# Optimization experiments

Measured on AMD Instinct MI355X. Metric: run time of the kernel, lower is better.

Reference implementation:

```python
import jax, jax.numpy as jnp
import numpy as np

N = 50000
E = 400000
IN_DIM = 384
HID = 256
Q_DIM = 384
HEAD_HID = 128


def _glorot(key, shape):
    fan_in, fan_out = shape[0], shape[1]
    lim = float(np.sqrt(6.0 / (fan_in + fan_out)))
    return jax.random.uniform(key, shape, jnp.float32, -lim, lim)


def setup_inputs() -> dict:
    key = jax.random.key(0)
    ks = jax.random.split(key, 10)
    x = jax.random.normal(ks[0], (N, IN_DIM), jnp.float32)
    edge_index = jax.random.randint(ks[1], (2, E), 0, N, dtype=jnp.int64)
    q = jax.random.normal(ks[2], (Q_DIM,), jnp.float32)
    # layer 1: Linear(in_dim*2 + query_dim -> hidden)
    W1 = _glorot(ks[3], (IN_DIM * 2 + Q_DIM, HID))
    b1 = jnp.zeros((HID,), jnp.float32)
    # layer 2: Linear(hidden*2 + query_dim -> hidden)
    W2 = _glorot(ks[4], (HID * 2 + Q_DIM, HID))
    b2 = jnp.zeros((HID,), jnp.float32)
    # score head: Linear(hidden + query_dim -> 128) -> ReLU -> Linear(128 -> 1)
    Wh1 = _glorot(ks[5], (HID + Q_DIM, HEAD_HID))
    bh1 = jnp.zeros((HEAD_HID,), jnp.float32)
    Wh2 = _glorot(ks[6], (HEAD_HID, 1))
    bh2 = jnp.zeros((1,), jnp.float32)
    return {"x": x, "edge_index": edge_index, "q": q,
            "W1": W1, "b1": b1, "W2": W2, "b2": b2,
            "Wh1": Wh1, "bh1": bh1, "Wh2": Wh2, "bh2": bh2}


def _sage_layer(h, src, dst, q, W, b, n_nodes):
    # mean aggregation with self-loops: (sum_{j in N(i)} h_j + h_i) / (deg_i + 1)
    deg = jnp.zeros((n_nodes,), h.dtype).at[dst].add(1.0) + 1.0  # [N]
    agg = (jax.ops.segment_sum(h[src], dst, num_segments=n_nodes) + h) / deg[:, None]
    q_exp = jnp.broadcast_to(q, (n_nodes, q.shape[0]))
    cat = jnp.concatenate([h, agg, q_exp], axis=-1)  # [N, 2*d + q_dim]
    return jax.nn.relu(cat @ W + b)  # dropout is identity in eval mode


def reference(x, edge_index, q, W1, b1, W2, b2, Wh1, bh1, Wh2, bh2):
    src, dst = edge_index[0], edge_index[1]
    n = x.shape[0]
    h = _sage_layer(x, src, dst, q, W1, b1, n)
    h = _sage_layer(h, src, dst, q, W2, b2, n)
    q_exp = jnp.broadcast_to(q, (n, q.shape[0]))
    s = jax.nn.relu(jnp.concatenate([h, q_exp], axis=-1) @ Wh1 + bh1)
    logits = (s @ Wh2 + bh2).squeeze(-1)  # [N]
    return logits
```

## Files before the change

kernel.cpp:

```cpp
#include <hip/hip_runtime.h>
#include <cstdint>
#include <cstddef>

typedef unsigned short u16;
typedef short short8 __attribute__((ext_vector_type(8)));
typedef unsigned short u16x8 __attribute__((ext_vector_type(8)));
typedef unsigned short u16x4 __attribute__((ext_vector_type(4)));
typedef float f32x4 __attribute__((ext_vector_type(4)));

#define DEVI __device__ __forceinline__

#if defined(__has_builtin)
#if __has_builtin(__builtin_amdgcn_global_load_lds)
#define USE_GLD 1
#endif
#endif

DEVI float bf2f(u16 u) { return __uint_as_float(((unsigned)u) << 16); }
DEVI u16 f2bf(float f) {
  unsigned u = __float_as_uint(f);
  u += 0x7FFFu + ((u >> 16) & 1u);
  return (u16)(u >> 16);
}

DEVI void stage16(const u16* __restrict__ g, u16* lds_base, int lane) {
#ifdef USE_GLD
  __builtin_amdgcn_global_load_lds(
      (const __attribute__((address_space(1))) unsigned int*)g,
      (__attribute__((address_space(3))) unsigned int*)lds_base, 16, 0, 0);
#else
  *(u16x8*)(lds_base + lane * 8) = *(const u16x8*)g;
#endif
}

__global__ void build_deg(const int* __restrict__ dst, int* __restrict__ deg, int E) {
  int e = blockIdx.x * 256 + threadIdx.x;
  if (e < E) atomicAdd(&deg[dst[e]], 1);
}

__global__ __launch_bounds__(256) void scan1(const int* __restrict__ deg,
                                             int* __restrict__ pref,
                                             int* __restrict__ bsum, int Nn) {
  __shared__ int wsum[4];
  int i = blockIdx.x * 256 + threadIdx.x;
  int lane = threadIdx.x & 63, w = threadIdx.x >> 6;
  int v = (i < Nn) ? deg[i] : 0;
  int s = v;
  for (int off = 1; off < 64; off <<= 1) {
    int t = __shfl_up(s, off, 64);
    if (lane >= off) s += t;
  }
  if (lane == 63) wsum[w] = s;
  __syncthreads();
  int add = 0;
  for (int k = 0; k < w; ++k) add += wsum[k];
  int incl = s + add;
  if (i < Nn) pref[i] = incl - v;
  if (threadIdx.x == 255) bsum[blockIdx.x] = incl;
}

__global__ __launch_bounds__(256) void scan2(int* __restrict__ bsum,
                                             int* __restrict__ row_ofs,
                                             int nb, int Nn) {
  __shared__ int wsum[4];
  int t = threadIdx.x;
  int lane = t & 63, w = t >> 6;
  int v = (t < nb) ? bsum[t] : 0;
  int s = v;
  for (int off = 1; off < 64; off <<= 1) {
    int u = __shfl_up(s, off, 64);
    if (lane >= off) s += u;
  }
  if (lane == 63) wsum[w] = s;
  __syncthreads();
  int add = 0;
  for (int k = 0; k < w; ++k) add += wsum[k];
  int incl = s + add;
  if (t < nb) bsum[t] = incl - v;
  if (t == 255) row_ofs[Nn] = incl;
}

__global__ __launch_bounds__(256) void scan3(const int* __restrict__ pref,
                                             const int* __restrict__ bsum,
                                             int* __restrict__ row_ofs,
                                             int* __restrict__ cursor, int Nn) {
  int i = blockIdx.x * 256 + threadIdx.x;
  if (i < Nn) {
    int r = pref[i] + bsum[blockIdx.x];
    row_ofs[i] = r;
    cursor[i] = r;
  }
}

__global__ void csr_fill(const int* __restrict__ src, const int* __restrict__ dst,
                         int* __restrict__ cursor, int* __restrict__ col, int E) {
  int e = blockIdx.x * 256 + threadIdx.x;
  if (e < E) {
    int p = atomicAdd(&cursor[dst[e]], 1);
    col[p] = src[e];
  }
}

__global__ __launch_bounds__(256) void pack_all(
    const float* __restrict__ W1, const float* __restrict__ W2,
    const float* __restrict__ Wh1, u16* __restrict__ B1t,
    u16* __restrict__ B2t, u16* __restrict__ Bht) {
  int b = blockIdx.x;
  if (b < 1024) {
    int c = b >> 1;
    int k = (b & 1) * 256 + threadIdx.x;
    if (k < 384) {
      float v = (c < 256) ? W1[(size_t)k * 256 + c]
                          : W1[(size_t)(384 + k) * 256 + (c - 256)];
      B1t[(size_t)c * 384 + k] = f2bf(v);
    }
  } else if (b < 1536) {
    int c = b - 1024;
    int k = threadIdx.x;
    float v = (c < 256) ? W2[(size_t)k * 256 + c]
                        : W2[(size_t)(256 + k) * 256 + (c - 256)];
    B2t[(size_t)c * 256 + k] = f2bf(v);
  } else {
    int c = b - 1536;
    int k = threadIdx.x;
    Bht[(size_t)c * 256 + k] = f2bf(Wh1[(size_t)k * 128 + c]);
  }
}

__global__ __launch_bounds__(384) void bias_all(
    const float* __restrict__ W1, const float* __restrict__ b1,
    const float* __restrict__ W2, const float* __restrict__ b2,
    const float* __restrict__ Wh1, const float* __restrict__ bh1,
    const float* __restrict__ q, float* __restrict__ cq1,
    float* __restrict__ cq2, float* __restrict__ cqh) {
  __shared__ float part[6];
  int b = blockIdx.x;
  const float* W; const float* bb; float* o; int ld, roff, c;
  if (b < 256)      { W = W1;  bb = b1;  o = cq1; ld = 256; roff = 768; c = b; }
  else if (b < 512) { W = W2;  bb = b2;  o = cq2; ld = 256; roff = 512; c = b - 256; }
  else              { W = Wh1; bb = bh1; o = cqh; ld = 128; roff = 256; c = b - 512; }
  int t = threadIdx.x;
  float p = q[t] * W[(size_t)(roff + t) * ld + c];
  for (int off = 32; off > 0; off >>= 1) p += __shfl_down(p, off, 64);
  if ((t & 63) == 0) part[t >> 6] = p;
  __syncthreads();
  if (t == 0) {
    float acc = bb[c];
    for (int w = 0; w < 6; ++w) acc += part[w];
    o[c] = acc;
  }
}

#define W_NC 512
#define ES 520
#define OFF_A0 0
#define OFF_A1 (64 * 32)
#define OFF_B0 (2 * 64 * 32)
#define OFF_B1 (2 * 64 * 32 + 512 * 32)
#define SMEM_TOT (2 * 64 * 32 + 2 * 512 * 32)

#define GEMM512_COMPUTE(LA, LB)                                                \
  {                                                                            \
    short8 bfr[8];                                                             \
    _Pragma("unroll") for (int nt = 0; nt < 8; ++nt) bfr[nt] =                 \
        *(const short8*)&(LB)[((wave * 128 + nt * 16 + m) * 4 + csel) * 8];    \
    _Pragma("unroll") for (int mt = 0; mt < 4; ++mt) {                         \
      short8 af = *(const short8*)&(LA)[((mt * 16 + m) * 4 + csel) * 8];       \
      _Pragma("unroll") for (int nt = 0; nt < 8; ++nt)                         \
          acc[mt][nt] = __builtin_amdgcn_mfma_f32_16x16x32_bf16(               \
              af, bfr[nt], acc[mt][nt], 0, 0, 0);                              \
    }                                                                          \
  }

#define GEMM512_EPILOGUE()                                                     \
  {                                                                            \
    u16* et = lds_b0;                                                          \
    _Pragma("unroll") for (int mt = 0; mt < 4; ++mt) {                         \
      __syncthreads();                                                         \
      _Pragma("unroll") for (int nt = 0; nt < 8; ++nt) {                       \
        int col = wave * 128 + nt * 16 + m;                                    \
        float bb = (col < bias_len) ? bias[col] : 0.0f;                        \
        _Pragma("unroll") for (int r = 0; r < 4; ++r) {                        \
          float v = acc[mt][nt][r] + bb;                                       \
          if (relu) v = fmaxf(v, 0.0f);                                        \
          et[(quad * 4 + r) * ES + col] = f2bf(v);                             \
        }                                                                      \
      }                                                                        \
      __syncthreads();                                                         \
      _Pragma("unroll") for (int p = 0; p < 4; ++p) {                          \
        int row_loc = p * 4 + wave;                                            \
        int grow = row0 + mt * 16 + row_loc;                                   \
        if (grow < M)                                                          \
          *(u16x8*)&C[(size_t)grow * W_NC + lane * 8] =                        \
              *(const u16x8*)&et[row_loc * ES + lane * 8];                     \
      }                                                                        \
    }                                                                          \
  }

#define GEMM512_B_SETUP()                                                      \
  const u16* pbB[8];                                                           \
  _Pragma("unroll") for (int p = 0; p < 8; ++p) {                              \
    int L = p * 256 + tid;                                                     \
    int c = L >> 2, qs = L & 3;                                                \
    int g = qs ^ ((c >> 1) & 3);                                               \
    pbB[p] = Bt + (size_t)c * K + g * 8;                                       \
  }

#define GEMM512_B_STAGE2()                                                     \
  _Pragma("unroll") for (int p = 0; p < 8; ++p) {                              \
    u16* d = lds_b0 + (size_t)(p * 256 + wave * 64) * 8;                       \
    stage16(pbB[p], d, lane);                                                  \
    stage16(pbB[p] + 32, d + (512 * 32), lane);         \
    pbB[p] += 64;                                                              \
  }

__global__ __launch_bounds__(256, 2) void gemm512_f32a(
    const float* __restrict__ A, const u16* __restrict__ Bt,
    u16* __restrict__ C, const float* __restrict__ bias,
    int M, int K, int bias_len, int relu) {
  __shared__ __align__(16) u16 smem[SMEM_TOT];
  u16* lds_a0 = smem + OFF_A0;
  u16* lds_a1 = smem + OFF_A1;
  u16* lds_b0 = smem + OFF_B0;
  u16* lds_b1 = smem + OFF_B1;

  const int tid = threadIdx.x;
  const int lane = tid & 63;
  const int wave = tid >> 6;
  const int row0 = blockIdx.x * 64;
  const int m = lane & 15;
  const int quad = lane >> 4;
  const int csel = quad ^ ((m >> 1) & 3);

  const int rA = tid >> 2;
  const int qA = tid & 3;
  const int sA = rA * 4 + (qA ^ ((rA >> 1) & 3));
  int ga = row0 + rA; if (ga >= M) ga = M - 1;
  const float* pa = A + (size_t)ga * K + qA * 8;

  GEMM512_B_SETUP()

  f32x4 acc[4][8] = {};

  f32x4 v0a = *(const f32x4*)pa, v0b = *(const f32x4*)(pa + 4);
  f32x4 v1a = *(const f32x4*)(pa + 32), v1b = *(const f32x4*)(pa + 36);
  pa += 64;

  for (int k0 = 0; k0 < K; k0 += 64) {
    __syncthreads();
    GEMM512_B_STAGE2()
    u16x8 h0, h1;
#pragma unroll
    for (int j = 0; j < 4; ++j) {
      h0[j] = f2bf(v0a[j]); h0[j + 4] = f2bf(v0b[j]);
      h1[j] = f2bf(v1a[j]); h1[j + 4] = f2bf(v1b[j]);
    }
    *(u16x8*)&lds_a0[sA * 8] = h0;
    *(u16x8*)&lds_a1[sA * 8] = h1;
    const float* pn = (k0 + 64 < K) ? pa : A;
    f32x4 n0a = *(const f32x4*)pn, n0b = *(const f32x4*)(pn + 4);
    f32x4 n1a = *(const f32x4*)(pn + 32), n1b = *(const f32x4*)(pn + 36);
    pa += 64;
    __syncthreads();
    GEMM512_COMPUTE(lds_a0, lds_b0)
    GEMM512_COMPUTE(lds_a1, lds_b1)
    v0a = n0a; v0b = n0b; v1a = n1a; v1b = n1b;
  }

  GEMM512_EPILOGUE()
}

__global__ __launch_bounds__(256, 2) void gemm512_bf16a(
    const u16* __restrict__ A, const u16* __restrict__ Bt,
    u16* __restrict__ C, const float* __restrict__ bias,
    int M, int K, int bias_len, int relu) {
  __shared__ __align__(16) u16 smem[SMEM_TOT];
  u16* lds_a0 = smem + OFF_A0;
  u16* lds_a1 = smem + OFF_A1;
  u16* lds_b0 = smem + OFF_B0;
  u16* lds_b1 = smem + OFF_B1;

  const int tid = threadIdx.x;
  const int lane = tid & 63;
  const int wave = tid >> 6;
  const int row0 = blockIdx.x * 64;
  const int m = lane & 15;
  const int quad = lane >> 4;
  const int csel = quad ^ ((m >> 1) & 3);

  const int rA = tid >> 2;
  const int qA = tid & 3;
  const int sA = rA * 4 + (qA ^ ((rA >> 1) & 3));
  int ga = row0 + rA; if (ga >= M) ga = M - 1;
  const u16* pa = A + (size_t)ga * K + qA * 8;

  GEMM512_B_SETUP()

  f32x4 acc[4][8] = {};

  u16x8 va0 = *(const u16x8*)pa;
  u16x8 va1 = *(const u16x8*)(pa + 32);
  pa += 64;

  for (int k0 = 0; k0 < K; k0 += 64) {
    __syncthreads();
    GEMM512_B_STAGE2()
    *(u16x8*)&lds_a0[sA * 8] = va0;
    *(u16x8*)&lds_a1[sA * 8] = va1;
    const u16* pn = (k0 + 64 < K) ? pa : A;
    u16x8 na0 = *(const u16x8*)pn;
    u16x8 na1 = *(const u16x8*)(pn + 32);
    pa += 64;
    __syncthreads();
    GEMM512_COMPUTE(lds_a0, lds_b0)
    GEMM512_COMPUTE(lds_a1, lds_b1)
    va0 = na0; va1 = na1;
  }

  GEMM512_EPILOGUE()
}

#define BM 128
#define BK 32

__global__ __launch_bounds__(256) void gemm_head(
    const u16* __restrict__ A, const u16* __restrict__ Bt,
    const float* __restrict__ cqh, const float* __restrict__ Wh2,
    const float* __restrict__ bh2, float* __restrict__ out, int M, int K) {
  __shared__ __align__(16) u16 lds_a[BM * BK];
  __shared__ __align__(16) u16 lds_b[BM * BK];
  __shared__ float red[128][2];

  const int tid = threadIdx.x;
  const int lane = tid & 63;
  const int wave = tid >> 6;
  const int wm = wave & 1, wn = wave >> 1;
  const int row0 = blockIdx.x * BM;
  const int m = lane & 15;
  const int quad = lane >> 4;
  const int csel = quad ^ ((m >> 1) & 3);

  const int r0 = tid >> 2, r1 = 64 + r0;
  const int cs = tid & 3;
  const int s0 = r0 * 4 + (cs ^ ((r0 >> 1) & 3));
  const int s1 = r1 * 4 + (cs ^ ((r1 >> 1) & 3));
  const int cb0 = cs ^ ((r0 >> 1) & 3);
  const int cb1 = cs ^ ((r1 >> 1) & 3);
  int ga0 = row0 + r0; if (ga0 >= M) ga0 = M - 1;
  int ga1 = row0 + r1; if (ga1 >= M) ga1 = M - 1;
  const u16* pa0 = A + (size_t)ga0 * K + cs * 8;
  const u16* pa1 = A + (size_t)ga1 * K + cs * 8;
  const u16* pb0 = Bt + (size_t)r0 * K + cb0 * 8;
  const u16* pb1 = Bt + (size_t)r1 * K + cb1 * 8;
  u16* lb0 = lds_b + (size_t)(wave * 64) * 8;
  u16* lb1 = lds_b + (size_t)(256 + wave * 64) * 8;

  f32x4 acc[4][4] = {};

  u16x8 va0 = *(const u16x8*)pa0; pa0 += BK;
  u16x8 va1 = *(const u16x8*)pa1; pa1 += BK;

  for (int k0 = 0; k0 < K; k0 += BK) {
    __syncthreads();
    stage16(pb0, lb0, lane); pb0 += BK;
    stage16(pb1, lb1, lane); pb1 += BK;
    *(u16x8*)&lds_a[s0 * 8] = va0;
    *(u16x8*)&lds_a[s1 * 8] = va1;
    const u16* n0 = (k0 + BK < K) ? pa0 : A;
    const u16* n1 = (k0 + BK < K) ? pa1 : A;
    u16x8 w0 = *(const u16x8*)n0;
    u16x8 w1 = *(const u16x8*)n1;
    pa0 += BK; pa1 += BK;
    __syncthreads();

    short8 af[4], bfv[4];
#pragma unroll
    for (int mt = 0; mt < 4; ++mt)
      af[mt] = *(const short8*)&lds_a[((wm * 64 + mt * 16 + m) * 4 + csel) * 8];
#pragma unroll
    for (int nt = 0; nt < 4; ++nt)
      bfv[nt] = *(const short8*)&lds_b[((wn * 64 + nt * 16 + m) * 4 + csel) * 8];
#pragma unroll
    for (int mt = 0; mt < 4; ++mt)
#pragma unroll
      for (int nt = 0; nt < 4; ++nt)
        acc[mt][nt] = __builtin_amdgcn_mfma_f32_16x16x32_bf16(
            af[mt], bfv[nt], acc[mt][nt], 0, 0, 0);
    va0 = w0; va1 = w1;
  }

  float part[4][4];
#pragma unroll
  for (int mt = 0; mt < 4; ++mt)
#pragma unroll
    for (int r = 0; r < 4; ++r) part[mt][r] = 0.0f;
#pragma unroll
  for (int nt = 0; nt < 4; ++nt) {
    int col = wn * 64 + nt * 16 + m;
    float bb = cqh[col];
    float w2 = Wh2[col];
#pragma unroll
    for (int mt = 0; mt < 4; ++mt)
#pragma unroll
      for (int r = 0; r < 4; ++r)
        part[mt][r] += fmaxf(acc[mt][nt][r] + bb, 0.0f) * w2;
  }
#pragma unroll
  for (int off = 8; off > 0; off >>= 1)
#pragma unroll
    for (int mt = 0; mt < 4; ++mt)
#pragma unroll
      for (int r = 0; r < 4; ++r)
        part[mt][r] += __shfl_xor(part[mt][r], off, 64);
  if (m == 0) {
#pragma unroll
    for (int mt = 0; mt < 4; ++mt)
#pragma unroll
      for (int r = 0; r < 4; ++r)
        red[wm * 64 + mt * 16 + quad * 4 + r][wn] = part[mt][r];
  }
  __syncthreads();
  if (tid < 128) {
    int grow = row0 + tid;
    if (grow < M) out[grow] = red[tid][0] + red[tid][1] + bh2[0];
  }
}

__global__ __launch_bounds__(256) void aggregate(
    const u16* __restrict__ C, const int* __restrict__ row_ofs,
    const int* __restrict__ col_idx, u16* __restrict__ H, int Nn) {
  int node = blockIdx.x * 4 + (threadIdx.x >> 6);
  if (node >= Nn) return;
  int lane = threadIdx.x & 63;
  int s = row_ofs[node], e = row_ofs[node + 1];
  float inv = 1.0f / (float)(e - s + 1);
  const u16* crow = C + (size_t)node * 512;
  u16x4 y0 = *(const u16x4*)(crow + 256 + lane * 4);
  float a0 = bf2f(y0[0]), a1 = bf2f(y0[1]), a2 = bf2f(y0[2]), a3 = bf2f(y0[3]);
  int t = s;
  for (; t + 4 <= e; t += 4) {
    int j0 = col_idx[t], j1 = col_idx[t + 1], j2 = col_idx[t + 2], j3 = col_idx[t + 3];
    u16x4 v0 = *(const u16x4*)(C + (size_t)j0 * 512 + 256 + lane * 4);
    u16x4 v1 = *(const u16x4*)(C + (size_t)j1 * 512 + 256 + lane * 4);
    u16x4 v2 = *(const u16x4*)(C + (size_t)j2 * 512 + 256 + lane * 4);
    u16x4 v3 = *(const u16x4*)(C + (size_t)j3 * 512 + 256 + lane * 4);
    a0 += bf2f(v0[0]) + bf2f(v1[0]) + bf2f(v2[0]) + bf2f(v3[0]);
    a1 += bf2f(v0[1]) + bf2f(v1[1]) + bf2f(v2[1]) + bf2f(v3[1]);
    a2 += bf2f(v0[2]) + bf2f(v1[2]) + bf2f(v2[2]) + bf2f(v3[2]);
    a3 += bf2f(v0[3]) + bf2f(v1[3]) + bf2f(v2[3]) + bf2f(v3[3]);
  }
  for (; t < e; ++t) {
    int j = col_idx[t];
    u16x4 yj = *(const u16x4*)(C + (size_t)j * 512 + 256 + lane * 4);
    a0 += bf2f(yj[0]); a1 += bf2f(yj[1]); a2 += bf2f(yj[2]); a3 += bf2f(yj[3]);
  }
  u16x4 u = *(const u16x4*)(crow + lane * 4);
  u16x4 o;
  o[0] = f2bf(fmaxf(bf2f(u[0]) + a0 * inv, 0.0f));
  o[1] = f2bf(fmaxf(bf2f(u[1]) + a1 * inv, 0.0f));
  o[2] = f2bf(fmaxf(bf2f(u[2]) + a2 * inv, 0.0f));
  o[3] = f2bf(fmaxf(bf2f(u[3]) + a3 * inv, 0.0f));
  *(u16x4*)(H + (size_t)node * 256 + lane * 4) = o;
}

extern "C" void kernel_launch(void* const* d_in, const int* in_sizes, int n_in,
                              void* d_out, int out_size, void* d_ws, size_t ws_size,
                              hipStream_t stream) {
  const float* x   = (const float*)d_in[0];
  const int*   ei  = (const int*)d_in[1];
  const float* q   = (const float*)d_in[2];
  const float* W1  = (const float*)d_in[3];
  const float* b1  = (const float*)d_in[4];
  const float* W2  = (const float*)d_in[5];
  const float* b2  = (const float*)d_in[6];
  const float* Wh1 = (const float*)d_in[7];
  const float* bh1 = (const float*)d_in[8];
  const float* Wh2 = (const float*)d_in[9];
  const float* bh2 = (const float*)d_in[10];

  const int N = in_sizes[0] / 384;
  const int E = in_sizes[1] / 2;
  const int Npad = ((N + 127) / 128) * 128;
  const int* esrc = ei;
  const int* edst = ei + E;

  size_t off = 0;
  auto alloc = [&](size_t bytes) -> void* {
    void* p = (char*)d_ws + off;
    off += (bytes + 255) & ~(size_t)255;
    return p;
  };
  int* deg     = (int*)alloc((size_t)N * 4);
  int* row_ofs = (int*)alloc((size_t)(N + 1) * 4);
  int* cursor  = (int*)alloc((size_t)N * 4);
  int* colidx  = (int*)alloc((size_t)E * 4);
  int* pref    = (int*)alloc((size_t)N * 4);
  int* bsum    = (int*)alloc(256 * 4);
  u16* B1t = (u16*)alloc((size_t)512 * 384 * 2);
  u16* B2t = (u16*)alloc((size_t)512 * 256 * 2);
  u16* Bht = (u16*)alloc((size_t)128 * 256 * 2);
  float* cq1 = (float*)alloc(256 * 4);
  float* cq2 = (float*)alloc(256 * 4);
  float* cqh = (float*)alloc(128 * 4);
  u16* Cbuf = (u16*)alloc((size_t)Npad * 512 * 2);
  u16* Hbuf = (u16*)alloc((size_t)Npad * 256 * 2);

  (void)hipMemsetAsync(deg, 0, (size_t)N * 4, stream);
  int eb = (E + 255) / 256;
  int nb = (N + 255) / 256;
  build_deg<<<eb, 256, 0, stream>>>(edst, deg, E);
  scan1<<<nb, 256, 0, stream>>>(deg, pref, bsum, N);
  scan2<<<1, 256, 0, stream>>>(bsum, row_ofs, nb, N);
  scan3<<<nb, 256, 0, stream>>>(pref, bsum, row_ofs, cursor, N);
  csr_fill<<<eb, 256, 0, stream>>>(esrc, edst, cursor, colidx, E);

  pack_all<<<1664, 256, 0, stream>>>(W1, W2, Wh1, B1t, B2t, Bht);
  bias_all<<<640, 384, 0, stream>>>(W1, b1, W2, b2, Wh1, bh1, q, cq1, cq2, cqh);

  int gb64 = (N + 63) / 64;
  int mb = Npad / 128;
  int nb4 = (N + 3) / 4;
  gemm512_f32a<<<gb64, 256, 0, stream>>>(x, B1t, Cbuf, cq1, N, 384, 256, 0);
  aggregate<<<nb4, 256, 0, stream>>>(Cbuf, row_ofs, colidx, Hbuf, N);
  gemm512_bf16a<<<gb64, 256, 0, stream>>>(Hbuf, B2t, Cbuf, cq2, N, 256, 256, 0);
  aggregate<<<nb4, 256, 0, stream>>>(Cbuf, row_ofs, colidx, Hbuf, N);
  gemm_head<<<mb, 256, 0, stream>>>(Hbuf, Bht, cqh, Wh2, bh2, (float*)d_out, N, 256);
}
```

Measured before the change: 345.9 us.

## Load MFMA operands directly from global memory, bypassing LDS staging in GEMMs

All three GEMM kernels stop staging A and B tiles through shared memory with double-buffered barriers. Each lane now loads its MFMA fragments straight from global memory (B from the small packed weight matrix, A rows per lane), and LDS is used only for the epilogue transpose. This removes the LDS writes, LDS reads and per-iteration __syncthreads, but each wave now fetches A redundantly through L1/L2. Every lane reads 16-byte pieces scattered across rows, so loads are less coalesced and global latency is less well hidden.

```diff
diff --git a/kernel.cpp b/kernel.cpp
--- a/kernel.cpp
+++ b/kernel.cpp
@@ -153,28 +153,9 @@
 
 #define W_NC 512
 #define ES 520
-#define OFF_A0 0
-#define OFF_A1 (64 * 32)
-#define OFF_B0 (2 * 64 * 32)
-#define OFF_B1 (2 * 64 * 32 + 512 * 32)
-#define SMEM_TOT (2 * 64 * 32 + 2 * 512 * 32)
-
-#define GEMM512_COMPUTE(LA, LB)                                                \
+
+#define GEMM_DIR_EPILOGUE()                                                    \
   {                                                                            \
-    short8 bfr[8];                                                             \
-    _Pragma("unroll") for (int nt = 0; nt < 8; ++nt) bfr[nt] =                 \
-        *(const short8*)&(LB)[((wave * 128 + nt * 16 + m) * 4 + csel) * 8];    \
-    _Pragma("unroll") for (int mt = 0; mt < 4; ++mt) {                         \
-      short8 af = *(const short8*)&(LA)[((mt * 16 + m) * 4 + csel) * 8];       \
-      _Pragma("unroll") for (int nt = 0; nt < 8; ++nt)                         \
-          acc[mt][nt] = __builtin_amdgcn_mfma_f32_16x16x32_bf16(               \
-              af, bfr[nt], acc[mt][nt], 0, 0, 0);                              \
-    }                                                                          \
-  }
-
-#define GEMM512_EPILOGUE()                                                     \
-  {                                                                            \
-    u16* et = lds_b0;                                                          \
     _Pragma("unroll") for (int mt = 0; mt < 4; ++mt) {                         \
       __syncthreads();                                                         \
       _Pragma("unroll") for (int nt = 0; nt < 8; ++nt) {                       \
@@ -183,7 +164,7 @@
         _Pragma("unroll") for (int r = 0; r < 4; ++r) {                        \
           float v = acc[mt][nt][r] + bb;                                       \
           if (relu) v = fmaxf(v, 0.0f);                                        \
-          et[(quad * 4 + r) * ES + col] = f2bf(v);                             \
+          eplds[(quad * 4 + r) * ES + col] = f2bf(v);                          \
         }                                                                      \
       }                                                                        \
       __syncthreads();                                                         \
@@ -192,37 +173,16 @@
         int grow = row0 + mt * 16 + row_loc;                                   \
         if (grow < M)                                                          \
           *(u16x8*)&C[(size_t)grow * W_NC + lane * 8] =                        \
-              *(const u16x8*)&et[row_loc * ES + lane * 8];                     \
+              *(const u16x8*)&eplds[row_loc * ES + lane * 8];                  \
       }                                                                        \
     }                                                                          \
   }
 
-#define GEMM512_B_SETUP()                                                      \
-  const u16* pbB[8];                                                           \
-  _Pragma("unroll") for (int p = 0; p < 8; ++p) {                              \
-    int L = p * 256 + tid;                                                     \
-    int c = L >> 2, qs = L & 3;                                                \
-    int g = qs ^ ((c >> 1) & 3);                                               \
-    pbB[p] = Bt + (size_t)c * K + g * 8;                                       \
-  }
-
-#define GEMM512_B_STAGE2()                                                     \
-  _Pragma("unroll") for (int p = 0; p < 8; ++p) {                              \
-    u16* d = lds_b0 + (size_t)(p * 256 + wave * 64) * 8;                       \
-    stage16(pbB[p], d, lane);                                                  \
-    stage16(pbB[p] + 32, d + (512 * 32), lane);         \
-    pbB[p] += 64;                                                              \
-  }
-
-__global__ __launch_bounds__(256, 2) void gemm512_f32a(
+__global__ __launch_bounds__(256, 2) void gemm_dir_f32a(
     const float* __restrict__ A, const u16* __restrict__ Bt,
     u16* __restrict__ C, const float* __restrict__ bias,
     int M, int K, int bias_len, int relu) {
-  __shared__ __align__(16) u16 smem[SMEM_TOT];
-  u16* lds_a0 = smem + OFF_A0;
-  u16* lds_a1 = smem + OFF_A1;
-  u16* lds_b0 = smem + OFF_B0;
-  u16* lds_b1 = smem + OFF_B1;
+  __shared__ __align__(16) u16 eplds[16 * ES];
 
   const int tid = threadIdx.x;
   const int lane = tid & 63;
@@ -230,55 +190,53 @@
   const int row0 = blockIdx.x * 64;
   const int m = lane & 15;
   const int quad = lane >> 4;
-  const int csel = quad ^ ((m >> 1) & 3);
-
-  const int rA = tid >> 2;
-  const int qA = tid & 3;
-  const int sA = rA * 4 + (qA ^ ((rA >> 1) & 3));
-  int ga = row0 + rA; if (ga >= M) ga = M - 1;
-  const float* pa = A + (size_t)ga * K + qA * 8;
-
-  GEMM512_B_SETUP()
+
+  const float* pa[4];
+#pragma unroll
+  for (int mt = 0; mt < 4; ++mt) {
+    int r = row0 + mt * 16 + m;
+    if (r >= M) r = M - 1;
+    pa[mt] = A + (size_t)r * K + quad * 8;
+  }
+  const u16* pb[8];
+#pragma unroll
+  for (int nt = 0; nt < 8; ++nt)
+    pb[nt] = Bt + (size_t)(wave * 128 + nt * 16 + m) * K + quad * 8;
 
   f32x4 acc[4][8] = {};
 
-  f32x4 v0a = *(const f32x4*)pa, v0b = *(const f32x4*)(pa + 4);
-  f32x4 v1a = *(const f32x4*)(pa + 32), v1b = *(const f32x4*)(pa + 36);
-  pa += 64;
-
-  for (int k0 = 0; k0 < K; k0 += 64) {
-    __syncthreads();
-    GEMM512_B_STAGE2()
-    u16x8 h0, h1;
-#pragma unroll
-    for (int j = 0; j < 4; ++j) {
-      h0[j] = f2bf(v0a[j]); h0[j + 4] = f2bf(v0b[j]);
-      h1[j] = f2bf(v1a[j]); h1[j + 4] = f2bf(v1b[j]);
+#pragma unroll 2
+  for (int k0 = 0; k0 < K; k0 += 32) {
+    short8 bf[8];
+#pragma unroll
+    for (int nt = 0; nt < 8; ++nt)
+      bf[nt] = *(const short8*)(pb[nt] + k0);
+    short8 af[4];
+#pragma unroll
+    for (int mt = 0; mt < 4; ++mt) {
+      f32x4 a0 = *(const f32x4*)(pa[mt] + k0);
+      f32x4 a1 = *(const f32x4*)(pa[mt] + k0 + 4);
+      u16x8 h;
+#pragma unroll
+      for (int j = 0; j < 4; ++j) { h[j] = f2bf(a0[j]); h[j + 4] = f2bf(a1[j]); }
+      af[mt] = *(short8*)&h;
     }
-    *(u16x8*)&lds_a0[sA * 8] = h0;
-    *(u16x8*)&lds_a1[sA * 8] = h1;
-    const float* pn = (k0 + 64 < K) ? pa : A;
-    f32x4 n0a = *(const f32x4*)pn, n0b = *(const f32x4*)(pn + 4);
-    f32x4 n1a = *(const f32x4*)(pn + 32), n1b = *(const f32x4*)(pn + 36);
-    pa += 64;
-    __syncthreads();
-    GEMM512_COMPUTE(lds_a0, lds_b0)
-    GEMM512_COMPUTE(lds_a1, lds_b1)
-    v0a = n0a; v0b = n0b; v1a = n1a; v1b = n1b;
-  }
-
-  GEMM512_EPILOGUE()
-}
-
-__global__ __launch_bounds__(256, 2) void gemm512_bf16a(
+#pragma unroll
+    for (int mt = 0; mt < 4; ++mt)
+#pragma unroll
+      for (int nt = 0; nt < 8; ++nt)
+        acc[mt][nt] = __builtin_amdgcn_mfma_f32_16x16x32_bf16(
+            af[mt], bf[nt], acc[mt][nt], 0, 0, 0);
+  }
+
+  GEMM_DIR_EPILOGUE()
+}
+
+__global__ __launch_bounds__(256, 2) void gemm_dir_bf16a(
     const u16* __restrict__ A, const u16* __restrict__ Bt,
     u16* __restrict__ C, const float* __restrict__ bias,
     int M, int K, int bias_len, int relu) {
-  __shared__ __align__(16) u16 smem[SMEM_TOT];
-  u16* lds_a0 = smem + OFF_A0;
-  u16* lds_a1 = smem + OFF_A1;
-  u16* lds_b0 = smem + OFF_B0;
-  u16* lds_b1 = smem + OFF_B1;
+  __shared__ __align__(16) u16 eplds[16 * ES];
 
   const int tid = threadIdx.x;
   const int lane = tid & 63;
@@ -286,38 +244,40 @@
   const int row0 = blockIdx.x * 64;
   const int m = lane & 15;
   const int quad = lane >> 4;
-  const int csel = quad ^ ((m >> 1) & 3);
-
-  const int rA = tid >> 2;
-  const int qA = tid & 3;
-  const int sA = rA * 4 + (qA ^ ((rA >> 1) & 3));
-  int ga = row0 + rA; if (ga >= M) ga = M - 1;
-  const u16* pa = A + (size_t)ga * K + qA * 8;
-
-  GEMM512_B_SETUP()
+
+  const u16* pa[4];
+#pragma unroll
+  for (int mt = 0; mt < 4; ++mt) {
+    int r = row0 + mt * 16 + m;
+    if (r >= M) r = M - 1;
+    pa[mt] = A + (size_t)r * K + quad * 8;
+  }
+  const u16* pb[8];
+#pragma unroll
+  for (int nt = 0; nt < 8; ++nt)
+    pb[nt] = Bt + (size_t)(wave * 128 + nt * 16 + m) * K + quad * 8;
 
   f32x4 acc[4][8] = {};
 
-  u16x8 va0 = *(const u16x8*)pa;
-  u16x8 va1 = *(const u16x8*)(pa + 32);
-  pa += 64;
-
-  for (int k0 = 0; k0 < K; k0 += 64) {
-    __syncthreads();
-    GEMM512_B_STAGE2()
-    *(u16x8*)&lds_a0[sA * 8] = va0;
-    *(u16x8*)&lds_a1[sA * 8] = va1;
-    const u16* pn = (k0 + 64 < K) ? pa : A;
-    u16x8 na0 = *(const u16x8*)pn;
-    u16x8 na1 = *(const u16x8*)(pn + 32);
-    pa += 64;
-    __syncthreads();
-    GEMM512_COMPUTE(lds_a0, lds_b0)
-    GEMM512_COMPUTE(lds_a1, lds_b1)
-    va0 = na0; va1 = na1;
-  }
-
-  GEMM512_EPILOGUE()
+#pragma unroll 2
+  for (int k0 = 0; k0 < K; k0 += 32) {
+    short8 bf[8];
+#pragma unroll
+    for (int nt = 0; nt < 8; ++nt)
+      bf[nt] = *(const short8*)(pb[nt] + k0);
+    short8 af[4];
+#pragma unroll
+    for (int mt = 0; mt < 4; ++mt)
+      af[mt] = *(const short8*)(pa[mt] + k0);
+#pragma unroll
+    for (int mt = 0; mt < 4; ++mt)
+#pragma unroll
+      for (int nt = 0; nt < 8; ++nt)
+        acc[mt][nt] = __builtin_amdgcn_mfma_f32_16x16x32_bf16(
+            af[mt], bf[nt], acc[mt][nt], 0, 0, 0);
+  }
+
+  GEMM_DIR_EPILOGUE()
 }
 
 #define BM 128
@@ -327,8 +287,6 @@
     const u16* __restrict__ A, const u16* __restrict__ Bt,
     const float* __restrict__ cqh, const float* __restrict__ Wh2,
     const float* __restrict__ bh2, float* __restrict__ out, int M, int K) {
-  __shared__ __align__(16) u16 lds_a[BM * BK];
-  __shared__ __align__(16) u16 lds_b[BM * BK];
   __shared__ float red[128][2];
 
   const int tid = threadIdx.x;
@@ -338,55 +296,34 @@
   const int row0 = blockIdx.x * BM;
   const int m = lane & 15;
   const int quad = lane >> 4;
-  const int csel = quad ^ ((m >> 1) & 3);
-
-  const int r0 = tid >> 2, r1 = 64 + r0;
-  const int cs = tid & 3;
-  const int s0 = r0 * 4 + (cs ^ ((r0 >> 1) & 3));
-  const int s1 = r1 * 4 + (cs ^ ((r1 >> 1) & 3));
-  const int cb0 = cs ^ ((r0 >> 1) & 3);
-  const int cb1 = cs ^ ((r1 >> 1) & 3);
-  int ga0 = row0 + r0; if (ga0 >= M) ga0 = M - 1;
-  int ga1 = row0 + r1; if (ga1 >= M) ga1 = M - 1;
-  const u16* pa0 = A + (size_t)ga0 * K + cs * 8;
-  const u16* pa1 = A + (size_t)ga1 * K + cs * 8;
-  const u16* pb0 = Bt + (size_t)r0 * K + cb0 * 8;
-  const u16* pb1 = Bt + (size_t)r1 * K + cb1 * 8;
-  u16* lb0 = lds_b + (size_t)(wave * 64) * 8;
-  u16* lb1 = lds_b + (size_t)(256 + wave * 64) * 8;
+
+  const u16* pa[4];
+#pragma unroll
+  for (int mt = 0; mt < 4; ++mt) {
+    int r = row0 + wm * 64 + mt * 16 + m;
+    if (r >= M) r = M - 1;
+    pa[mt] = A + (size_t)r * K + quad * 8;
+  }
+  const u16* pb[4];
+#pragma unroll
+  for (int nt = 0; nt < 4; ++nt)
+    pb[nt] = Bt + (size_t)(wn * 64 + nt * 16 + m) * K + quad * 8;
 
   f32x4 acc[4][4] = {};
 
-  u16x8 va0 = *(const u16x8*)pa0; pa0 += BK;
-  u16x8 va1 = *(const u16x8*)pa1; pa1 += BK;
-
+#pragma unroll 2
   for (int k0 = 0; k0 < K; k0 += BK) {
-    __syncthreads();
-    stage16(pb0, lb0, lane); pb0 += BK;
-    stage16(pb1, lb1, lane); pb1 += BK;
-    *(u16x8*)&lds_a[s0 * 8] = va0;
-    *(u16x8*)&lds_a[s1 * 8] = va1;
-    const u16* n0 = (k0 + BK < K) ? pa0 : A;
-    const u16* n1 = (k0 + BK < K) ? pa1 : A;
-    u16x8 w0 = *(const u16x8*)n0;
-    u16x8 w1 = *(const u16x8*)n1;
-    pa0 += BK; pa1 += BK;
-    __syncthreads();
-
-    short8 af[4], bfv[4];
-#pragma unroll
-    for (int mt = 0; mt < 4; ++mt)
-      af[mt] = *(const short8*)&lds_a[((wm * 64 + mt * 16 + m) * 4 + csel) * 8];
-#pragma unroll
-    for (int nt = 0; nt < 4; ++nt)
-      bfv[nt] = *(const short8*)&lds_b[((wn * 64 + nt * 16 + m) * 4 + csel) * 8];
+    short8 bf[4], af[4];
+#pragma unroll
+    for (int nt = 0; nt < 4; ++nt) bf[nt] = *(const short8*)(pb[nt] + k0);
+#pragma unroll
+    for (int mt = 0; mt < 4; ++mt) af[mt] = *(const short8*)(pa[mt] + k0);
 #pragma unroll
     for (int mt = 0; mt < 4; ++mt)
 #pragma unroll
       for (int nt = 0; nt < 4; ++nt)
         acc[mt][nt] = __builtin_amdgcn_mfma_f32_16x16x32_bf16(
-            af[mt], bfv[nt], acc[mt][nt], 0, 0, 0);
-    va0 = w0; va1 = w1;
+            af[mt], bf[nt], acc[mt][nt], 0, 0, 0);
   }
 
   float part[4][4];
@@ -520,9 +457,9 @@
   int gb64 = (N + 63) / 64;
   int mb = Npad / 128;
   int nb4 = (N + 3) / 4;
-  gemm512_f32a<<<gb64, 256, 0, stream>>>(x, B1t, Cbuf, cq1, N, 384, 256, 0);
+  gemm_dir_f32a<<<gb64, 256, 0, stream>>>(x, B1t, Cbuf, cq1, N, 384, 256, 0);
   aggregate<<<nb4, 256, 0, stream>>>(Cbuf, row_ofs, colidx, Hbuf, N);
-  gemm512_bf16a<<<gb64, 256, 0, stream>>>(Hbuf, B2t, Cbuf, cq2, N, 256, 256, 0);
+  gemm_dir_bf16a<<<gb64, 256, 0, stream>>>(Hbuf, B2t, Cbuf, cq2, N, 256, 256, 0);
   aggregate<<<nb4, 256, 0, stream>>>(Cbuf, row_ofs, colidx, Hbuf, N);
   gemm_head<<<mb, 256, 0, stream>>>(Hbuf, Bht, cqh, Wh2, bh2, (float*)d_out, N, 256);
 }
```

Measured after the change: 434.5 us. +25.6%, slower.
